# Kernel tuning notes

Measured on AMD Instinct MI355X. Metric: run time of the kernel, lower is better.

The kernel has to match this reference:

```python
import jax, jax.numpy as jnp
import numpy as np

B, C, H, W = 32, 512, 24, 8
C8 = C // 8  # PAM query/key channels


def setup_inputs() -> dict:
    key = jax.random.key(0)
    k0, k1, k2, k3, k4 = jax.random.split(key, 5)
    x = jax.random.normal(k0, (B, C, H, W), dtype=jnp.float32)
    Wq = jax.random.normal(k1, (C8, C), dtype=jnp.float32) * 0.02
    bq = jnp.zeros((C8,), dtype=jnp.float32)
    Wk = jax.random.normal(k2, (C8, C), dtype=jnp.float32) * 0.02
    bk = jnp.zeros((C8,), dtype=jnp.float32)
    return {"x": x, "Wq": Wq, "bq": bq, "Wk": Wk, "bk": bk}


def reference(x, Wq, bq, Wk, bk):
    b, c, h, w = x.shape
    hw = h * w
    xf = x.reshape(b, c, hw)  # [B, C, hw]

    # QAConv: einsum('gchw,pcyx->gpyxhw') with kernel == x, then view(B,-1,hw,hw).
    # With m=(h,w) of features and n=(y,x) of kernel this is 'gcm,pcn->gpnm'.
    score = jnp.einsum('gcm,pcn->gpnm', xf, xf)  # [B, B, hw, hw]
    kernel_max = score.max(axis=3)               # max over feature positions -> [B, B, hw]

    # PAM: 1x1 conv projections then bmm(q^T, k).
    q = jnp.einsum('qc,bcm->bqm', Wq, xf) + bq[None, :, None]  # [B, C8, hw]
    k = jnp.einsum('qc,bcm->bqm', Wk, xf) + bk[None, :, None]  # [B, C8, hw]
    energy = jnp.einsum('bqm,bqn->bmn', q, k)                  # [B, hw, hw]
    pos_max = energy.max(axis=2)[None]                         # [1, B, hw]

    return jnp.concatenate([kernel_max, pos_max], axis=0)  # [B+1, B, hw]
```

## Files before the change

### kernel.cpp

```cpp
#include <hip/hip_runtime.h>

typedef __bf16 bf16x8 __attribute__((ext_vector_type(8)));
typedef float f32x4 __attribute__((ext_vector_type(4)));
typedef unsigned short u16x8 __attribute__((ext_vector_type(8)));
typedef unsigned short u16x4 __attribute__((ext_vector_type(4)));

#define B_ 32
#define CC 512
#define HW 192
#define C8_ 64
#define NTRI 528
#define NG2 1056
#define BUF_B 36864
#define SMEM_BYTES 73728

__device__ inline unsigned short f2bf(float f) {
    unsigned u = __float_as_uint(f);
    unsigned r = (u + 0x7FFFu + ((u >> 16) & 1u)) >> 16;
    return (unsigned short)r;
}

__device__ inline void gload16(const void* g, void* l) {
    __builtin_amdgcn_global_load_lds(
        (const __attribute__((address_space(1))) unsigned*)g,
        (__attribute__((address_space(3))) unsigned*)l,
        16, 0, 0);
}

__global__ void prep(const float* __restrict__ x,
                     const float* __restrict__ Wq, const float* __restrict__ Wk,
                     unsigned short* __restrict__ xt,
                     unsigned short* __restrict__ wqb, unsigned short* __restrict__ wkb) {
    __shared__ unsigned short tile[64 * 64];
    int t = threadIdx.x;
    if (blockIdx.x >= 96) {
        int id = (blockIdx.x - 96) * 8 + blockIdx.y;
        const float* src = (id < 32) ? Wq : Wk;
        unsigned short* dst = (id < 32) ? wqb : wkb;
        int base = (id & 31) * 1024 + t * 4;
        f32x4 a = *(const f32x4*)(src + base);
        u16x4 o;
        #pragma unroll
        for (int e = 0; e < 4; ++e) o[e] = f2bf(a[e]);
        *(u16x4*)(dst + base) = o;
        return;
    }
    int b = blockIdx.x / 3, mt = blockIdx.x % 3;
    int m0 = mt * 64, c0 = blockIdx.y * 64;
    const float* xb = x + (size_t)b * CC * HW + (size_t)c0 * HW + m0;

    int mq = t & 15, cl0 = t >> 4;
    int sw = (mq & 7) << 3;
    #pragma unroll
    for (int rd = 0; rd < 4; ++rd) {
        int cl = rd * 16 + cl0;
        f32x4 v = *(const f32x4*)(xb + cl * HW + mq * 4);
        #pragma unroll
        for (int e = 0; e < 4; ++e)
            tile[(mq * 4 + e) * 64 + (cl ^ sw)] = f2bf(v[e]);
    }
    __syncthreads();
    unsigned short* xo = xt + ((size_t)b * HW + m0) * CC + c0;
    int kc = t & 7, mr0 = t >> 3;
    #pragma unroll
    for (int rd = 0; rd < 2; ++rd) {
        int mr = rd * 32 + mr0;
        u16x8 v = *(const u16x8*)&tile[mr * 64 + ((kc << 3) ^ (((mr >> 2) & 7) << 3))];
        *(u16x8*)(xo + (size_t)mr * CC + kc * 8) = v;
    }
}

__global__ __launch_bounds__(256) void pam_qk(
        const unsigned short* __restrict__ xt,
        const unsigned short* __restrict__ wqb, const unsigned short* __restrict__ wkb,
        const float* __restrict__ bq, const float* __restrict__ bk,
        unsigned short* __restrict__ qo, unsigned short* __restrict__ ko) {
    int b = blockIdx.x, m0 = blockIdx.y * 48;
    int tid = threadIdx.x, w = tid >> 6, lane = tid & 63;
    int l15 = lane & 15, lq = lane >> 4;
    int qc = w * 16 + l15;

    f32x4 accq[3], acck[3];
    #pragma unroll
    for (int i = 0; i < 3; ++i) {
        accq[i] = (f32x4){0.f, 0.f, 0.f, 0.f};
        acck[i] = (f32x4){0.f, 0.f, 0.f, 0.f};
    }

    const unsigned short* xb = xt + ((size_t)b * HW + m0) * CC;
    const unsigned short* wqp = wqb + (size_t)qc * CC;
    const unsigned short* wkp = wkb + (size_t)qc * CC;

    for (int kt = 0; kt < 16; ++kt) {
        int ko8 = kt * 32 + lq * 8;
        bf16x8 wqf = *(const bf16x8*)(wqp + ko8);
        bf16x8 wkf = *(const bf16x8*)(wkp + ko8);
        bf16x8 af[3];
        #pragma unroll
        for (int i = 0; i < 3; ++i)
            af[i] = *(const bf16x8*)(xb + (i * 16 + l15) * CC + ko8);
        #pragma unroll
        for (int i = 0; i < 3; ++i) {
            accq[i] = __builtin_amdgcn_mfma_f32_16x16x32_bf16(af[i], wqf, accq[i], 0, 0, 0);
            acck[i] = __builtin_amdgcn_mfma_f32_16x16x32_bf16(af[i], wkf, acck[i], 0, 0, 0);
        }
    }

    float bqv = bq[qc], bkv = bk[qc];
    #pragma unroll
    for (int i = 0; i < 3; ++i) {
        #pragma unroll
        for (int r = 0; r < 4; ++r) {
            int m = m0 + i * 16 + lq * 4 + r;
            qo[((size_t)b * HW + m) * C8_ + qc] = f2bf(accq[i][r] + bqv);
            ko[((size_t)b * HW + m) * C8_ + qc] = f2bf(acck[i][r] + bkv);
        }
    }
}

__global__ __launch_bounds__(512, 4) void gram2(const unsigned short* __restrict__ xt,
                                                float* __restrict__ out,
                                                float* __restrict__ ws2) {
    extern __shared__ char smem[];

    int tid = threadIdx.x;
    int bid = (blockIdx.x & 7) * 132 + (blockIdx.x >> 3);
    int pairid = bid >> 1, h = bid & 1;
    int idx = pairid, g = 0;
    while (idx >= B_ - g) { idx -= B_ - g; ++g; }
    int p = g + idx;

    const unsigned short* xga = xt + ((size_t)g * HW + 96 * h) * CC;
    const unsigned short* xp  = xt + (size_t)p * HW * CC;

    int w = tid >> 6, lane = tid & 63;
    int wr = w >> 2, wc = w & 3;
    int l15 = lane & 15, lq = lane >> 4;

    const unsigned short* sp[5];
    unsigned lo[5];
    #pragma unroll
    for (int ci = 0; ci < 5; ++ci) {
        int R = (ci < 4) ? (w + 8 * ci) : (32 + w);
        int q = R * 64 + lane;
        if (ci == 4 && w >= 4) q = lane;
        lo[ci] = (unsigned)q * 16;
        if (q < 768) {
            int r = q >> 3, s = q & 7;
            sp[ci] = xga + r * CC + ((s ^ (r & 7)) << 3);
        } else {
            int q2 = q - 768, n = q2 >> 3, s = q2 & 7;
            sp[ci] = xp + n * CC + ((s ^ (n & 7)) << 3);
        }
    }

    unsigned aoff[3], boff[3];
    #pragma unroll
    for (int i = 0; i < 3; ++i) {
        int row = wr * 48 + i * 16 + l15;
        aoff[i] = (unsigned)row * 128 + ((unsigned)(lq ^ (row & 7)) << 4);
    }
    #pragma unroll
    for (int j = 0; j < 3; ++j) {
        int n = wc * 48 + j * 16 + l15;
        boff[j] = 12288u + (unsigned)n * 128 + ((unsigned)(lq ^ (n & 7)) << 4);
    }

    f32x4 acc[3][3];
    #pragma unroll
    for (int i = 0; i < 3; ++i)
        #pragma unroll
        for (int j = 0; j < 3; ++j)
            acc[i][j] = (f32x4){0.f, 0.f, 0.f, 0.f};

    #define STG2(buf, kt)                                                      \
        {                                                                      \
            char* base = smem + (buf) * BUF_B;                                 \
            int k0 = (kt) * 64;                                                \
            gload16(sp[0] + k0, base + lo[0]);                                 \
            gload16(sp[1] + k0, base + lo[1]);                                 \
            gload16(sp[2] + k0, base + lo[2]);                                 \
            gload16(sp[3] + k0, base + lo[3]);                                 \
            if (w < 4) gload16(sp[4] + k0, base + lo[4]);                      \
        }

    #define CMP2(buf)                                                          \
        {                                                                      \
            const char* Bb = smem + (buf) * BUF_B;                             \
            _Pragma("unroll")                                                  \
            for (int kx = 0; kx < 128; kx += 64) {                             \
                bf16x8 af[3], bfr[3];                                          \
                _Pragma("unroll")                                              \
                for (int i = 0; i < 3; ++i)                                    \
                    af[i] = *(const bf16x8*)(Bb + (aoff[i] ^ kx));             \
                _Pragma("unroll")                                              \
                for (int j = 0; j < 3; ++j)                                    \
                    bfr[j] = *(const bf16x8*)(Bb + (boff[j] ^ kx));            \
                _Pragma("unroll")                                              \
                for (int i = 0; i < 3; ++i)                                    \
                    _Pragma("unroll")                                          \
                    for (int j = 0; j < 3; ++j)                                \
                        acc[i][j] = __builtin_amdgcn_mfma_f32_16x16x32_bf16(   \
                            af[i], bfr[j], acc[i][j], 0, 0, 0);                \
            }                                                                  \
        }

    STG2(0, 0);
    __syncthreads();
    for (int kt = 0; kt < 8; ++kt) {
        int cur = kt & 1;
        if (kt < 7) STG2(cur ^ 1, kt + 1);
        CMP2(cur);
        __syncthreads();
    }

    float* rowbuf = (float*)smem;
    float* colbuf = (float*)(smem + 1536);

    #pragma unroll
    for (int i = 0; i < 3; ++i) {
        float rm[4];
        #pragma unroll
        for (int r = 0; r < 4; ++r) rm[r] = -1e30f;
        #pragma unroll
        for (int j = 0; j < 3; ++j)
            #pragma unroll
            for (int r = 0; r < 4; ++r)
                rm[r] = fmaxf(rm[r], acc[i][j][r]);
        #pragma unroll
        for (int msk = 1; msk <= 8; msk <<= 1)
            #pragma unroll
            for (int r = 0; r < 4; ++r)
                rm[r] = fmaxf(rm[r], __shfl_xor(rm[r], msk));
        if (l15 == 0) {
            #pragma unroll
            for (int r = 0; r < 4; ++r)
                rowbuf[wc * 96 + wr * 48 + i * 16 + lq * 4 + r] = rm[r];
        }
    }
    #pragma unroll
    for (int j = 0; j < 3; ++j) {
        float cm = -1e30f;
        #pragma unroll
        for (int i = 0; i < 3; ++i)
            #pragma unroll
            for (int r = 0; r < 4; ++r)
                cm = fmaxf(cm, acc[i][j][r]);
        cm = fmaxf(cm, __shfl_xor(cm, 16));
        cm = fmaxf(cm, __shfl_xor(cm, 32));
        if (lane < 16) colbuf[wr * HW + wc * 48 + j * 16 + l15] = cm;
    }
    __syncthreads();
    if (tid < 96) {
        float v = fmaxf(fmaxf(rowbuf[tid], rowbuf[96 + tid]),
                        fmaxf(rowbuf[192 + tid], rowbuf[288 + tid]));
        out[((size_t)p * B_ + g) * HW + 96 * h + tid] = v;
    }
    if (tid >= 128 && tid < 320) {
        int n = tid - 128;
        ws2[(size_t)pairid * 384 + h * 192 + n] = fmaxf(colbuf[n], colbuf[HW + n]);
    }
}

__global__ __launch_bounds__(256) void energy_fin(
        const unsigned short* __restrict__ qo,
        const unsigned short* __restrict__ ko,
        const float* __restrict__ ws2,
        float* __restrict__ out) {
    int tid = threadIdx.x;
    if (blockIdx.x >= 128) {
        int pairid = blockIdx.x - 128;
        int idx = pairid, g = 0;
        while (idx >= B_ - g) { idx -= B_ - g; ++g; }
        int p = g + idx;
        if (tid < HW)
            out[((size_t)g * B_ + p) * HW + tid] =
                fmaxf(ws2[(size_t)pairid * 384 + tid], ws2[(size_t)pairid * 384 + 192 + tid]);
        return;
    }
    int b = blockIdx.x >> 2, m0 = (blockIdx.x & 3) * 48;
    int w = tid >> 6, lane = tid & 63;
    int l15 = lane & 15, lq = lane >> 4;
    int n0 = w * 48;

    f32x4 acc[3][3];
    #pragma unroll
    for (int i = 0; i < 3; ++i)
        #pragma unroll
        for (int j = 0; j < 3; ++j)
            acc[i][j] = (f32x4){0.f, 0.f, 0.f, 0.f};

    const unsigned short* qb = qo + ((size_t)b * HW + m0) * C8_;
    const unsigned short* kb = ko + ((size_t)b * HW + n0) * C8_;

    #pragma unroll
    for (int kt = 0; kt < 2; ++kt) {
        int ko8 = kt * 32 + lq * 8;
        bf16x8 af[3], bfr[3];
        #pragma unroll
        for (int i = 0; i < 3; ++i)
            af[i] = *(const bf16x8*)(qb + (i * 16 + l15) * C8_ + ko8);
        #pragma unroll
        for (int j = 0; j < 3; ++j)
            bfr[j] = *(const bf16x8*)(kb + (j * 16 + l15) * C8_ + ko8);
        #pragma unroll
        for (int i = 0; i < 3; ++i)
            #pragma unroll
            for (int j = 0; j < 3; ++j)
                acc[i][j] = __builtin_amdgcn_mfma_f32_16x16x32_bf16(af[i], bfr[j], acc[i][j], 0, 0, 0);
    }

    __shared__ float red[4][48];
    #pragma unroll
    for (int i = 0; i < 3; ++i) {
        float rm[4];
        #pragma unroll
        for (int r = 0; r < 4; ++r) rm[r] = -1e30f;
        #pragma unroll
        for (int j = 0; j < 3; ++j)
            #pragma unroll
            for (int r = 0; r < 4; ++r)
                rm[r] = fmaxf(rm[r], acc[i][j][r]);
        #pragma unroll
        for (int msk = 1; msk <= 8; msk <<= 1)
            #pragma unroll
            for (int r = 0; r < 4; ++r)
                rm[r] = fmaxf(rm[r], __shfl_xor(rm[r], msk));
        if (l15 == 0) {
            #pragma unroll
            for (int r = 0; r < 4; ++r)
                red[w][i * 16 + lq * 4 + r] = rm[r];
        }
    }
    __syncthreads();
    if (tid < 48) {
        float v = fmaxf(fmaxf(red[0][tid], red[1][tid]),
                        fmaxf(red[2][tid], red[3][tid]));
        out[((size_t)B_ * B_ + b) * HW + m0 + tid] = v;
    }
}

extern "C" void kernel_launch(void* const* d_in, const int* in_sizes, int n_in,
                              void* d_out, int out_size, void* d_ws, size_t ws_size,
                              hipStream_t stream) {
    (void)in_sizes; (void)n_in; (void)out_size; (void)ws_size;
    const float* x  = (const float*)d_in[0];
    const float* Wq = (const float*)d_in[1];
    const float* bq = (const float*)d_in[2];
    const float* Wk = (const float*)d_in[3];
    const float* bk = (const float*)d_in[4];
    float* out = (float*)d_out;

    char* ws = (char*)d_ws;
    unsigned short* xt  = (unsigned short*)ws;
    unsigned short* wqb = (unsigned short*)(ws + 6291456);
    unsigned short* wkb = (unsigned short*)(ws + 6291456 + 65536);
    unsigned short* qbuf = (unsigned short*)(ws + 6291456 + 131072);
    unsigned short* kbuf = (unsigned short*)(ws + 6291456 + 131072 + 786432);
    float* ws2 = (float*)(ws + 6291456 + 131072 + 2 * 786432);

    hipFuncSetAttribute((const void*)gram2,
                        hipFuncAttributeMaxDynamicSharedMemorySize, SMEM_BYTES);

    prep<<<dim3(104, 8), dim3(256), 0, stream>>>(x, Wq, Wk, xt, wqb, wkb);
    pam_qk<<<dim3(32, 4), dim3(256), 0, stream>>>(xt, wqb, wkb, bq, bk, qbuf, kbuf);
    gram2<<<dim3(NG2), dim3(512), SMEM_BYTES, stream>>>(xt, out, ws2);
    energy_fin<<<dim3(656), dim3(256), 0, stream>>>(qbuf, kbuf, ws2, out);
}
```

Baseline: 56.38 us.

## Split gram tiles into 96x96 quadrants with smaller K-steps and static LDS

The gram kernel now gives each block one 96x96 quadrant of a batch-pair score matrix, using 256 threads instead of 512 and 2112 blocks. The K loop stages 32 channels per step (16 steps) into a 24KB static LDS double buffer with a new swizzle. All row and column partial maxima go to the workspace, and energy_fin combines the quadrants for both output orientations. The aim is higher occupancy and better load balance, at the cost of more K-loop barriers, more redundant global reads and extra reduction traffic.

```diff
diff --git a/kernel.cpp b/kernel.cpp
--- a/kernel.cpp
+++ b/kernel.cpp
@@ -10,9 +10,8 @@
 #define HW 192
 #define C8_ 64
 #define NTRI 528
-#define NG2 1056
-#define BUF_B 36864
-#define SMEM_BYTES 73728
+#define NG3 2112
+#define QBUF_B 12288
 
 __device__ inline unsigned short f2bf(float f) {
     unsigned u = __float_as_uint(f);
@@ -118,52 +117,45 @@
     }
 }
 
-__global__ __launch_bounds__(512, 4) void gram2(const unsigned short* __restrict__ xt,
-                                                float* __restrict__ out,
+__global__ __launch_bounds__(256, 5) void gram3(const unsigned short* __restrict__ xt,
                                                 float* __restrict__ ws2) {
-    extern __shared__ char smem[];
+    __shared__ __attribute__((aligned(16))) char smem[2 * QBUF_B];
 
     int tid = threadIdx.x;
-    int bid = (blockIdx.x & 7) * 132 + (blockIdx.x >> 3);
-    int pairid = bid >> 1, h = bid & 1;
+    int bid = (blockIdx.x & 7) * 264 + (blockIdx.x >> 3);
+    int pairid = bid >> 2, qi = (bid >> 1) & 1, qj = bid & 1;
     int idx = pairid, g = 0;
     while (idx >= B_ - g) { idx -= B_ - g; ++g; }
     int p = g + idx;
 
-    const unsigned short* xga = xt + ((size_t)g * HW + 96 * h) * CC;
-    const unsigned short* xp  = xt + (size_t)p * HW * CC;
+    const unsigned short* xga = xt + ((size_t)g * HW + 96 * qi) * CC;
+    const unsigned short* xpb = xt + ((size_t)p * HW + 96 * qj) * CC;
 
     int w = tid >> 6, lane = tid & 63;
-    int wr = w >> 2, wc = w & 3;
+    int wr = w >> 1, wc = w & 1;
     int l15 = lane & 15, lq = lane >> 4;
 
-    const unsigned short* sp[5];
-    unsigned lo[5];
-    #pragma unroll
-    for (int ci = 0; ci < 5; ++ci) {
-        int R = (ci < 4) ? (w + 8 * ci) : (32 + w);
-        int q = R * 64 + lane;
-        if (ci == 4 && w >= 4) q = lane;
+    const unsigned short* sp[3];
+    unsigned lo[3];
+    #pragma unroll
+    for (int ci = 0; ci < 3; ++ci) {
+        int q = tid + 256 * ci;
         lo[ci] = (unsigned)q * 16;
-        if (q < 768) {
-            int r = q >> 3, s = q & 7;
-            sp[ci] = xga + r * CC + ((s ^ (r & 7)) << 3);
-        } else {
-            int q2 = q - 768, n = q2 >> 3, s = q2 & 7;
-            sp[ci] = xp + n * CC + ((s ^ (n & 7)) << 3);
-        }
+        int q2 = (q < 384) ? q : q - 384;
+        int r = q2 >> 2, s = q2 & 3;
+        sp[ci] = ((q < 384) ? xga : xpb) + r * CC + (((s ^ ((r >> 1) & 3)) << 3));
     }
 
     unsigned aoff[3], boff[3];
     #pragma unroll
     for (int i = 0; i < 3; ++i) {
         int row = wr * 48 + i * 16 + l15;
-        aoff[i] = (unsigned)row * 128 + ((unsigned)(lq ^ (row & 7)) << 4);
+        aoff[i] = (unsigned)row * 64 + ((unsigned)(lq ^ ((row >> 1) & 3)) << 4);
     }
     #pragma unroll
     for (int j = 0; j < 3; ++j) {
         int n = wc * 48 + j * 16 + l15;
-        boff[j] = 12288u + (unsigned)n * 128 + ((unsigned)(lq ^ (n & 7)) << 4);
+        boff[j] = 6144u + (unsigned)n * 64 + ((unsigned)(lq ^ ((n >> 1) & 3)) << 4);
     }
 
     f32x4 acc[3][3];
@@ -173,49 +165,44 @@
         for (int j = 0; j < 3; ++j)
             acc[i][j] = (f32x4){0.f, 0.f, 0.f, 0.f};
 
-    #define STG2(buf, kt)                                                      \
+    #define STG3(buf, kt)                                                      \
         {                                                                      \
-            char* base = smem + (buf) * BUF_B;                                 \
-            int k0 = (kt) * 64;                                                \
+            char* base = smem + (buf) * QBUF_B;                                \
+            int k0 = (kt) * 32;                                                \
             gload16(sp[0] + k0, base + lo[0]);                                 \
             gload16(sp[1] + k0, base + lo[1]);                                 \
             gload16(sp[2] + k0, base + lo[2]);                                 \
-            gload16(sp[3] + k0, base + lo[3]);                                 \
-            if (w < 4) gload16(sp[4] + k0, base + lo[4]);                      \
-        }
-
-    #define CMP2(buf)                                                          \
+        }
+
+    #define CMP3(buf)                                                          \
         {                                                                      \
-            const char* Bb = smem + (buf) * BUF_B;                             \
+            const char* Bb = smem + (buf) * QBUF_B;                            \
+            bf16x8 af[3], bfr[3];                                              \
             _Pragma("unroll")                                                  \
-            for (int kx = 0; kx < 128; kx += 64) {                             \
-                bf16x8 af[3], bfr[3];                                          \
-                _Pragma("unroll")                                              \
-                for (int i = 0; i < 3; ++i)                                    \
-                    af[i] = *(const bf16x8*)(Bb + (aoff[i] ^ kx));             \
+            for (int i = 0; i < 3; ++i)                                        \
+                af[i] = *(const bf16x8*)(Bb + aoff[i]);                        \
+            _Pragma("unroll")                                                  \
+            for (int j = 0; j < 3; ++j)                                        \
+                bfr[j] = *(const bf16x8*)(Bb + boff[j]);                       \
+            _Pragma("unroll")                                                  \
+            for (int i = 0; i < 3; ++i)                                        \
                 _Pragma("unroll")                                              \
                 for (int j = 0; j < 3; ++j)                                    \
-                    bfr[j] = *(const bf16x8*)(Bb + (boff[j] ^ kx));            \
-                _Pragma("unroll")                                              \
-                for (int i = 0; i < 3; ++i)                                    \
-                    _Pragma("unroll")                                          \
-                    for (int j = 0; j < 3; ++j)                                \
-                        acc[i][j] = __builtin_amdgcn_mfma_f32_16x16x32_bf16(   \
-                            af[i], bfr[j], acc[i][j], 0, 0, 0);                \
-            }                                                                  \
-        }
-
-    STG2(0, 0);
+                    acc[i][j] = __builtin_amdgcn_mfma_f32_16x16x32_bf16(       \
+                        af[i], bfr[j], acc[i][j], 0, 0, 0);                    \
+        }
+
+    STG3(0, 0);
     __syncthreads();
-    for (int kt = 0; kt < 8; ++kt) {
+    for (int kt = 0; kt < 16; ++kt) {
         int cur = kt & 1;
-        if (kt < 7) STG2(cur ^ 1, kt + 1);
-        CMP2(cur);
+        if (kt < 15) STG3(cur ^ 1, kt + 1);
+        CMP3(cur);
         __syncthreads();
     }
 
-    float* rowbuf = (float*)smem;
-    float* colbuf = (float*)(smem + 1536);
+    float* rowred = (float*)smem;
+    float* colred = (float*)(smem + 768);
 
     #pragma unroll
     for (int i = 0; i < 3; ++i) {
@@ -235,7 +222,7 @@
         if (l15 == 0) {
             #pragma unroll
             for (int r = 0; r < 4; ++r)
-                rowbuf[wc * 96 + wr * 48 + i * 16 + lq * 4 + r] = rm[r];
+                rowred[wc * 96 + wr * 48 + i * 16 + lq * 4 + r] = rm[r];
         }
     }
     #pragma unroll
@@ -248,17 +235,15 @@
                 cm = fmaxf(cm, acc[i][j][r]);
         cm = fmaxf(cm, __shfl_xor(cm, 16));
         cm = fmaxf(cm, __shfl_xor(cm, 32));
-        if (lane < 16) colbuf[wr * HW + wc * 48 + j * 16 + l15] = cm;
+        if (lane < 16) colred[wr * 96 + wc * 48 + j * 16 + l15] = cm;
     }
     __syncthreads();
-    if (tid < 96) {
-        float v = fmaxf(fmaxf(rowbuf[tid], rowbuf[96 + tid]),
-                        fmaxf(rowbuf[192 + tid], rowbuf[288 + tid]));
-        out[((size_t)p * B_ + g) * HW + 96 * h + tid] = v;
-    }
-    if (tid >= 128 && tid < 320) {
-        int n = tid - 128;
-        ws2[(size_t)pairid * 384 + h * 192 + n] = fmaxf(colbuf[n], colbuf[HW + n]);
+    float* dst = ws2 + (size_t)(pairid * 4 + qi * 2 + qj) * 192;
+    if (tid < 96)
+        dst[tid] = fmaxf(rowred[tid], rowred[96 + tid]);
+    else if (tid < 192) {
+        int n = tid - 96;
+        dst[96 + n] = fmaxf(colred[n], colred[96 + n]);
     }
 }
 
@@ -273,9 +258,22 @@
         int idx = pairid, g = 0;
         while (idx >= B_ - g) { idx -= B_ - g; ++g; }
         int p = g + idx;
-        if (tid < HW)
-            out[((size_t)g * B_ + p) * HW + tid] =
-                fmaxf(ws2[(size_t)pairid * 384 + tid], ws2[(size_t)pairid * 384 + 192 + tid]);
+        const float* wp = ws2 + (size_t)pairid * 768;
+        #pragma unroll
+        for (int half = 0; half < 2; ++half) {
+            int k = half * 256 + tid;
+            if (k < 192) {
+                int j = k / 96, nn = k % 96;
+                out[((size_t)g * B_ + p) * HW + k] =
+                    fmaxf(wp[(0 * 2 + j) * 192 + 96 + nn],
+                          wp[(1 * 2 + j) * 192 + 96 + nn]);
+            } else if (k < 384) {
+                int m = k - 192, i = m / 96, mm = m % 96;
+                out[((size_t)p * B_ + g) * HW + m] =
+                    fmaxf(wp[(i * 2 + 0) * 192 + mm],
+                          wp[(i * 2 + 1) * 192 + mm]);
+            }
+        }
         return;
     }
     int b = blockIdx.x >> 2, m0 = (blockIdx.x & 3) * 48;
@@ -359,11 +357,8 @@
     unsigned short* kbuf = (unsigned short*)(ws + 6291456 + 131072 + 786432);
     float* ws2 = (float*)(ws + 6291456 + 131072 + 2 * 786432);
 
-    hipFuncSetAttribute((const void*)gram2,
-                        hipFuncAttributeMaxDynamicSharedMemorySize, SMEM_BYTES);
-
     prep<<<dim3(104, 8), dim3(256), 0, stream>>>(x, Wq, Wk, xt, wqb, wkb);
     pam_qk<<<dim3(32, 4), dim3(256), 0, stream>>>(xt, wqb, wkb, bq, bk, qbuf, kbuf);
-    gram2<<<dim3(NG2), dim3(512), SMEM_BYTES, stream>>>(xt, out, ws2);
+    gram3<<<dim3(NG3), dim3(256), 0, stream>>>(xt, ws2);
     energy_fin<<<dim3(656), dim3(256), 0, stream>>>(qbuf, kbuf, ws2, out);
 }
```

After: 60.50 us. 7.3% more time.
